# Optimization experiments

Measured on AMD Instinct MI355X. Metric: run time of the kernel, lower is better.

The kernel has to match this reference:

```python
import jax, jax.numpy as jnp
import numpy as np

B = 2          # batch size
T2 = 9         # temporal groups (b*t2 = grid_sample batch)
T3 = 27        # t1 // t2
T1 = 243       # t2 * t3
P = 17         # joints
K2 = 9         # kernel_size ** 2
C = 128        # dim_img
CH = [48, 96, 192, 384]
HW = [(96, 72), (48, 36), (24, 18), (12, 9)]
ALPHA = 0.9


def setup_inputs() -> dict:
    key = jax.random.key(0)
    ks = jax.random.split(key, 16)
    inp = {}
    N = B * T2
    for i, (c, (h, w)) in enumerate(zip(CH, HW)):
        inp[f"f{i}"] = jax.random.normal(ks[i], (N, c, h, w), jnp.float32)
    inp["query"] = jax.random.normal(ks[4], (B, T1, P * K2, C), jnp.float32)
    # key holds normalized grid coords in [-1, 1]
    inp["key"] = jax.random.uniform(ks[5], (N, T3, P * K2, 2), jnp.float32) * 2.0 - 1.0
    inp["value"] = jax.random.normal(ks[6], (B, T1, P, C), jnp.float32)
    s = 0.05
    inp["w_off"] = jax.random.normal(ks[7], (2, C), jnp.float32) * s
    inp["b_off"] = jnp.zeros((2,), jnp.float32)
    inp["w_attn"] = jax.random.normal(ks[8], (2, C), jnp.float32) * s
    inp["b_attn"] = jnp.zeros((2,), jnp.float32)
    for i, c in enumerate(CH):
        inp[f"we{i}"] = jax.random.normal(ks[9 + i], (C, c), jnp.float32) * s
        inp[f"be{i}"] = jnp.zeros((C,), jnp.float32)
    inp["conv_w"] = jax.random.normal(ks[13], (C, C, K2), jnp.float32) * s
    inp["conv_b"] = jnp.zeros((C,), jnp.float32)
    return inp


def _grid_sample(img, grid):
    """Bilinear grid_sample, align_corners=False, zero padding.
    img: [N, C, H, W]; grid: [N, Hg, Wg, 2] in [-1,1] (x=width, y=height).
    Returns [N, Hg, Wg, C] (channels-last for the following 1x1 conv)."""
    N, Cin, H, W = img.shape
    gx, gy = grid[..., 0], grid[..., 1]
    ix = ((gx + 1.0) * W - 1.0) * 0.5
    iy = ((gy + 1.0) * H - 1.0) * 0.5
    ix0 = jnp.floor(ix); iy0 = jnp.floor(iy)
    wx1 = ix - ix0; wx0 = 1.0 - wx1
    wy1 = iy - iy0; wy0 = 1.0 - wy1
    bidx = jnp.arange(N)[:, None, None]

    def gather(yy, xx):
        yi = yy.astype(jnp.int32); xi = xx.astype(jnp.int32)
        valid = (yi >= 0) & (yi < H) & (xi >= 0) & (xi < W)
        yc = jnp.clip(yi, 0, H - 1); xc = jnp.clip(xi, 0, W - 1)
        v = img[bidx, :, yc, xc]  # [N, Hg, Wg, C]
        return v * valid[..., None].astype(img.dtype)

    out = (gather(iy0, ix0) * (wy0 * wx0)[..., None]
           + gather(iy0, ix0 + 1.0) * (wy0 * wx1)[..., None]
           + gather(iy0 + 1.0, ix0) * (wy1 * wx0)[..., None]
           + gather(iy0 + 1.0, ix0 + 1.0) * (wy1 * wx1)[..., None])
    return out


def reference(f0, f1, f2, f3, query, key, value,
              w_off, b_off, w_attn, b_attn,
              we0, be0, we1, be1, we2, be2, we3, be3,
              conv_w, conv_b):
    b, t1, p, c = value.shape            # [B, 243, 17, 128]
    t3 = key.shape[1]                    # 27
    t2 = t1 // t3                        # 9

    # learned offsets per query location, squashed by tanh
    off = jnp.tanh(jnp.einsum('btqc,oc->btqo', query, w_off) + b_off)   # [b,t1,153,2]
    # per-joint softmax weights, tiled over the k^2 kernel taps
    aw = jax.nn.softmax(jnp.einsum('btpc,oc->btpo', value, w_attn) + b_attn, axis=-1)  # [b,t1,17,2]
    aw = jnp.tile(aw, (1, 1, K2, 1))                                     # [b,t1,153,2]

    sp = (off * aw).reshape(b * t2, t3, p * K2, 2)
    sampling_positions = key + sp                                        # [b*t2, 27, 153, 2]

    fmaps = (f0, f1, f2, f3)
    ws = (we0, we1, we2, we3)
    bs = (be0, be1, be2, be3)
    feats = []
    for f, w, bb in zip(fmaps, ws, bs):
        g = _grid_sample(f, sampling_positions)                          # [b*t2, 27, 153, C_in]
        e = jnp.einsum('nhwc,oc->nhwo', g, w) + bb                        # 1x1 conv embed -> 128
        feats.append(e.reshape(b, t2 * t3, p * K2, C))                    # [b, 243, 153, 128]
    new_query = jnp.mean(jnp.stack(feats, axis=-2), axis=-2)             # fuse 4 levels
    new_query = (1.0 - ALPHA) * new_query + ALPHA * query

    # grouped-by-position conv1d over the k^2 taps (full-width kernel -> length 1)
    x = new_query.reshape(b, t1, p, K2, c)                               # 'b t (p k) c'
    new_value = jnp.einsum('btpkc,ock->btpo', x, conv_w) + conv_b        # [b, 243, 17, 128]
    return (new_query, new_value, sampling_positions)
```

## Files before the change

kernel.cpp:

```cpp
#include <hip/hip_runtime.h>
#include <hip/hip_bf16.h>

static constexpr int NQ_SIZE = 9517824;
static constexpr int NV_SIZE = 1057536;
static constexpr int NPOS    = 74358;
static constexpr int M_CONV  = 8262;

static constexpr long E0_OFF = 0;
static constexpr long E1_OFF = 15925248;
static constexpr long E2_OFF = E1_OFF + 3981312;
static constexpr long E3_OFF = E2_OFF + 995328;
static constexpr long E_END  = E3_OFF + 248832;

static constexpr int SEG_F3  = 36;
static constexpr int SEG_F2  = SEG_F3 + 126;
static constexpr int SEG_F1  = SEG_F2 + 486;
static constexpr int SEG_F0  = SEG_F1 + 1944;
static constexpr int SEG_CT  = SEG_F0 + 576;
static constexpr int SEG_SP  = SEG_CT + 486;
static constexpr int PREP_GRID = SEG_SP;

typedef __attribute__((ext_vector_type(8))) short short8;
typedef __attribute__((ext_vector_type(4))) float floatx4;

__device__ __forceinline__ float bf2f(unsigned short u) {
    union { unsigned int i; float f; } v; v.i = ((unsigned)u) << 16; return v.f;
}
__device__ __forceinline__ unsigned short f2bf_rne(float f) {
    union { float f; unsigned int i; } v; v.f = f;
    unsigned int u = v.i;
    u += 0x7fffu + ((u >> 16) & 1u);
    return (unsigned short)(u >> 16);
}

__global__ __launch_bounds__(256) void prep_k(
    const float* __restrict__ f0, const float* __restrict__ f1,
    const float* __restrict__ f2, const float* __restrict__ f3,
    const float* __restrict__ we0, const float* __restrict__ we1,
    const float* __restrict__ we2, const float* __restrict__ we3,
    const float* __restrict__ conv_w, unsigned short* __restrict__ convT2,
    const float* __restrict__ query, const float* __restrict__ value,
    const float* __restrict__ key,
    const float* __restrict__ w_off, const float* __restrict__ b_off,
    const float* __restrict__ w_attn, const float* __restrict__ b_attn,
    float* __restrict__ samp, unsigned short* __restrict__ Ebase)
{
    const int bid = blockIdx.x;
    const int tid = threadIdx.x;

    if (bid < SEG_F0) {
        __shared__ unsigned short As[64][40];
        __shared__ unsigned short Bs[128][40];

        const float* A; const float* W; unsigned short* Eo;
        int M, K, m0;
        if (bid < SEG_F3) {
            int n = bid >> 1, t = bid & 1;
            M = 108; K = 384; A = f3 + (long)n * 384 * 108; W = we3;
            Eo = Ebase + E3_OFF + (long)n * 108 * 128; m0 = t * 64;
        } else if (bid < SEG_F2) {
            int r = bid - SEG_F3; int n = r / 7, t = r - n * 7;
            M = 432; K = 192; A = f2 + (long)n * 192 * 432; W = we2;
            Eo = Ebase + E2_OFF + (long)n * 432 * 128; m0 = t * 64;
        } else if (bid < SEG_F1) {
            int r = bid - SEG_F2; int n = r / 27, t = r - n * 27;
            M = 1728; K = 96; A = f1 + (long)n * 96 * 1728; W = we1;
            Eo = Ebase + E1_OFF + (long)n * 1728 * 128; m0 = t * 64;
        } else {
            int r = bid - SEG_F1; int n = r / 108, t = r - n * 108;
            M = 6912; K = 48; A = f0 + (long)n * 48 * 6912; W = we0;
            Eo = Ebase + E0_OFF + (long)n * 6912 * 128; m0 = t * 64;
        }

        const int lane = tid & 63;
        const int wave = tid >> 6;
        const int wm = (wave & 1) * 32;
        const int wn = (wave >> 1) * 64;
        const int l15  = lane & 15;
        const int quad = lane >> 4;

        floatx4 acc[2][4];
        #pragma unroll
        for (int i = 0; i < 2; ++i)
            #pragma unroll
            for (int j = 0; j < 4; ++j) acc[i][j] = (floatx4){0.f, 0.f, 0.f, 0.f};

        const int sak = tid >> 3;
        const int sam = (tid & 7) << 3;
        const int sbo = tid >> 1;
        const int sbk = (tid & 1) << 4;

        float4 av0, av1, bv0, bv1, bv2, bv3;
        auto fetch = [&](int k0) {
            av0 = (float4){0,0,0,0}; av1 = (float4){0,0,0,0};
            if (k0 + sak < K) {
                const float* p = A + (long)(k0 + sak) * M + m0 + sam;
                if (m0 + sam + 7 < M) {
                    av0 = *(const float4*)p;
                    av1 = *(const float4*)(p + 4);
                } else if (m0 + sam < M) {
                    float tmp[8] = {0,0,0,0,0,0,0,0};
                    int nv_ = M - (m0 + sam);
                    for (int i = 0; i < 8; ++i) if (i < nv_) tmp[i] = p[i];
                    av0 = (float4){tmp[0], tmp[1], tmp[2], tmp[3]};
                    av1 = (float4){tmp[4], tmp[5], tmp[6], tmp[7]};
                }
            }
            bv0 = (float4){0,0,0,0}; bv1 = bv0; bv2 = bv0; bv3 = bv0;
            if (k0 + sbk < K) {
                const float* wp = W + (long)sbo * K + k0 + sbk;
                bv0 = *(const float4*)wp;
                bv1 = *(const float4*)(wp + 4);
                bv2 = *(const float4*)(wp + 8);
                bv3 = *(const float4*)(wp + 12);
            }
        };
        fetch(0);

        for (int k0 = 0; k0 < K; k0 += 32) {
            {
                float tmp[8] = {av0.x, av0.y, av0.z, av0.w, av1.x, av1.y, av1.z, av1.w};
                #pragma unroll
                for (int i = 0; i < 8; ++i)
                    As[sam + i][sak] = f2bf_rne(tmp[i]);
            }
            {
                unsigned short t[16];
                float tmp[16] = {bv0.x, bv0.y, bv0.z, bv0.w, bv1.x, bv1.y, bv1.z, bv1.w,
                                 bv2.x, bv2.y, bv2.z, bv2.w, bv3.x, bv3.y, bv3.z, bv3.w};
                #pragma unroll
                for (int i = 0; i < 16; ++i) t[i] = f2bf_rne(tmp[i]);
                *(uint4*)&Bs[sbo][sbk]     = *(const uint4*)&t[0];
                *(uint4*)&Bs[sbo][sbk + 8] = *(const uint4*)&t[8];
            }
            __syncthreads();
            if (k0 + 32 < K) fetch(k0 + 32);

            short8 af[2], bfr[4];
            #pragma unroll
            for (int mt = 0; mt < 2; ++mt)
                af[mt] = *(const short8*)&As[wm + mt * 16 + l15][quad * 8];
            #pragma unroll
            for (int nt = 0; nt < 4; ++nt)
                bfr[nt] = *(const short8*)&Bs[wn + nt * 16 + l15][quad * 8];
            #pragma unroll
            for (int mt = 0; mt < 2; ++mt)
                #pragma unroll
                for (int nt = 0; nt < 4; ++nt)
                    acc[mt][nt] = __builtin_amdgcn_mfma_f32_16x16x32_bf16(
                        af[mt], bfr[nt], acc[mt][nt], 0, 0, 0);
            __syncthreads();
        }

        #pragma unroll
        for (int mt = 0; mt < 2; ++mt) {
            #pragma unroll
            for (int nt = 0; nt < 4; ++nt) {
                int col = wn + nt * 16 + l15;
                #pragma unroll
                for (int r = 0; r < 4; ++r) {
                    int m = m0 + wm + mt * 16 + quad * 4 + r;
                    if (m < M)
                        Eo[(long)m * 128 + col] = f2bf_rne(acc[mt][nt][r]);
                }
            }
        }
    } else if (bid < SEG_CT) {
        int idx = (bid - SEG_F0) * 256 + tid;
        if (idx < 147456) {
            int o = idx / 1152, kk = idx - o * 1152;
            int k2 = kk >> 7, c = kk & 127;
            convT2[idx] = f2bf_rne(conv_w[o * 1152 + c * 9 + k2]);
        }
    } else {
        const int bt1 = bid - SEG_CT;
        const int b  = bt1 / 243, t1 = bt1 - b * 243;
        const int t2 = t1 / 27,  t3 = t1 - t2 * 27;
        const int n  = b * 9 + t2;
        __shared__ float logit[17][2];
        __shared__ float aw[17][2];

        if (tid < 34) {
            int p = tid >> 1, o = tid & 1;
            const float* vrow = value + ((long)bt1 * 17 + p) * 128;
            const float* wrow = w_attn + o * 128;
            float s = 0.f;
            for (int c = 0; c < 128; c += 4) {
                float4 v = *(const float4*)(vrow + c);
                float4 w = *(const float4*)(wrow + c);
                s += v.x * w.x + v.y * w.y + v.z * w.z + v.w * w.w;
            }
            logit[p][o] = s + b_attn[o];
        }
        __syncthreads();
        if (tid < 17) {
            float l0 = logit[tid][0], l1 = logit[tid][1];
            float mx = fmaxf(l0, l1);
            float e0 = expf(l0 - mx), e1 = expf(l1 - mx);
            float inv = 1.f / (e0 + e1);
            aw[tid][0] = e0 * inv; aw[tid][1] = e1 * inv;
        }
        __syncthreads();
        for (int j = tid; j < 306; j += 256) {
            int q = j >> 1, o = j & 1;
            const float* qrow = query + ((long)bt1 * 153 + q) * 128;
            const float* wrow = w_off + o * 128;
            float s = 0.f;
            for (int c = 0; c < 128; c += 4) {
                float4 v = *(const float4*)(qrow + c);
                float4 w = *(const float4*)(wrow + c);
                s += v.x * w.x + v.y * w.y + v.z * w.z + v.w * w.w;
            }
            float off = tanhf(s + b_off[o]);
            float sp = off * aw[q % 17][o];
            long kidx = (((long)n * 27 + t3) * 153 + q) * 2 + o;
            samp[kidx] = key[kidx] + sp;
        }
    }
}

__global__ __launch_bounds__(256) void gather_k(
    const unsigned short* __restrict__ Ebase,
    const float* __restrict__ samp, const float* __restrict__ query,
    const float* __restrict__ be0, const float* __restrict__ be1,
    const float* __restrict__ be2, const float* __restrict__ be3,
    float* __restrict__ nq)
{
    const int tid = threadIdx.x;
    const int pos = blockIdx.x * 8 + (tid >> 5);
    if (pos >= NPOS) return;
    const int c4 = (tid & 31) << 2;
    const int bt1 = pos / 153, q = pos - bt1 * 153;
    const int b  = bt1 / 243, t1 = bt1 - b * 243;
    const int t2 = t1 / 27,  t3 = t1 - t2 * 27;
    const int n  = b * 9 + t2;
    const long sbase = (((long)n * 27 + t3) * 153 + q) * 2;
    const float gx = samp[sbase], gy = samp[sbase + 1];

    float ax = 0.f, ay = 0.f, az = 0.f, aww = 0.f;
    const long Eoffs[4] = {E0_OFF, E1_OFF, E2_OFF, E3_OFF};
    const int Hs[4] = {96, 48, 24, 12}, Wd[4] = {72, 36, 18, 9};
    #pragma unroll
    for (int l = 0; l < 4; ++l) {
        const int H = Hs[l], W = Wd[l];
        const unsigned short* E = Ebase + Eoffs[l] + (long)n * H * W * 128 + c4;
        float ix = ((gx + 1.f) * (float)W - 1.f) * 0.5f;
        float iy = ((gy + 1.f) * (float)H - 1.f) * 0.5f;
        float fx0 = floorf(ix), fy0 = floorf(iy);
        int x0 = (int)fx0, y0 = (int)fy0;
        int x1 = x0 + 1, y1 = y0 + 1;
        float wx1 = ix - fx0, wx0 = 1.f - wx1;
        float wy1 = iy - fy0, wy0 = 1.f - wy1;
        float w00 = wy0 * wx0, w01 = wy0 * wx1, w10 = wy1 * wx0, w11 = wy1 * wx1;
        bool vy0 = (unsigned)y0 < (unsigned)H, vy1 = (unsigned)y1 < (unsigned)H;
        bool vx0 = (unsigned)x0 < (unsigned)W, vx1 = (unsigned)x1 < (unsigned)W;
        if (vy0 && vx0) { ushort4 v = *(const ushort4*)(E + ((long)y0 * W + x0) * 128);
            ax = fmaf(w00, bf2f(v.x), ax); ay = fmaf(w00, bf2f(v.y), ay);
            az = fmaf(w00, bf2f(v.z), az); aww = fmaf(w00, bf2f(v.w), aww); }
        if (vy0 && vx1) { ushort4 v = *(const ushort4*)(E + ((long)y0 * W + x1) * 128);
            ax = fmaf(w01, bf2f(v.x), ax); ay = fmaf(w01, bf2f(v.y), ay);
            az = fmaf(w01, bf2f(v.z), az); aww = fmaf(w01, bf2f(v.w), aww); }
        if (vy1 && vx0) { ushort4 v = *(const ushort4*)(E + ((long)y1 * W + x0) * 128);
            ax = fmaf(w10, bf2f(v.x), ax); ay = fmaf(w10, bf2f(v.y), ay);
            az = fmaf(w10, bf2f(v.z), az); aww = fmaf(w10, bf2f(v.w), aww); }
        if (vy1 && vx1) { ushort4 v = *(const ushort4*)(E + ((long)y1 * W + x1) * 128);
            ax = fmaf(w11, bf2f(v.x), ax); ay = fmaf(w11, bf2f(v.y), ay);
            az = fmaf(w11, bf2f(v.z), az); aww = fmaf(w11, bf2f(v.w), aww); }
    }
    float bsx = be0[c4]     + be1[c4]     + be2[c4]     + be3[c4];
    float bsy = be0[c4 + 1] + be1[c4 + 1] + be2[c4 + 1] + be3[c4 + 1];
    float bsz = be0[c4 + 2] + be1[c4 + 2] + be2[c4 + 2] + be3[c4 + 2];
    float bsw = be0[c4 + 3] + be1[c4 + 3] + be2[c4 + 3] + be3[c4 + 3];
    float mx = 0.25f * (ax + bsx), my = 0.25f * (ay + bsy);
    float mz = 0.25f * (az + bsz), mw = 0.25f * (aww + bsw);
    const long qi = ((long)bt1 * 153 + q) * 128 + c4;
    float4 qv = *(const float4*)(query + qi);
    float4 o;
    o.x = 0.1f * mx + 0.9f * qv.x;
    o.y = 0.1f * my + 0.9f * qv.y;
    o.z = 0.1f * mz + 0.9f * qv.z;
    o.w = 0.1f * mw + 0.9f * qv.w;
    *(float4*)(nq + qi) = o;
}

__global__ __launch_bounds__(256) void conv_mfma_k(
    const float* __restrict__ nq, const unsigned short* __restrict__ convT2,
    const float* __restrict__ conv_b, float* __restrict__ nv)
{
    __shared__ unsigned short As[64][40];
    __shared__ unsigned short Bs[64][40];

    const int tid  = threadIdx.x;
    const int lane = tid & 63;
    const int wave = tid >> 6;
    const int wm = (wave & 1) * 32;
    const int wn = (wave >> 1) * 32;
    const int m0 = blockIdx.x * 64;
    const int n0 = blockIdx.y * 64;
    const int l15  = lane & 15;
    const int quad = lane >> 4;

    floatx4 acc[2][2];
    #pragma unroll
    for (int i = 0; i < 2; ++i)
        #pragma unroll
        for (int j = 0; j < 2; ++j) acc[i][j] = (floatx4){0.f, 0.f, 0.f, 0.f};

    const int am = tid >> 2;
    const int ak = (tid & 3) << 3;
    const int bn = tid & 63;
    const int bk = (tid >> 6) << 3;

    float4 a0, a1; uint4 bv;
    auto fetch = [&](int k0) {
        a0 = (float4){0,0,0,0}; a1 = (float4){0,0,0,0};
        int row = m0 + am;
        if (row < M_CONV) {
            const float* p = nq + (long)row * 1152 + k0 + ak;
            a0 = *(const float4*)p;
            a1 = *(const float4*)(p + 4);
        }
        bv = *(const uint4*)(convT2 + (long)(n0 + bn) * 1152 + k0 + bk);
    };
    fetch(0);

    for (int k0 = 0; k0 < 1152; k0 += 32) {
        unsigned short* dst = &As[am][ak];
        dst[0] = f2bf_rne(a0.x); dst[1] = f2bf_rne(a0.y);
        dst[2] = f2bf_rne(a0.z); dst[3] = f2bf_rne(a0.w);
        dst[4] = f2bf_rne(a1.x); dst[5] = f2bf_rne(a1.y);
        dst[6] = f2bf_rne(a1.z); dst[7] = f2bf_rne(a1.w);
        *(uint4*)&Bs[bn][bk] = bv;
        __syncthreads();
        if (k0 + 32 < 1152) fetch(k0 + 32);

        short8 af[2], bfr[2];
        #pragma unroll
        for (int mt = 0; mt < 2; ++mt)
            af[mt] = *(const short8*)&As[wm + mt * 16 + l15][quad * 8];
        #pragma unroll
        for (int nt = 0; nt < 2; ++nt)
            bfr[nt] = *(const short8*)&Bs[wn + nt * 16 + l15][quad * 8];
        #pragma unroll
        for (int mt = 0; mt < 2; ++mt)
            #pragma unroll
            for (int nt = 0; nt < 2; ++nt)
                acc[mt][nt] = __builtin_amdgcn_mfma_f32_16x16x32_bf16(
                    af[mt], bfr[nt], acc[mt][nt], 0, 0, 0);
        __syncthreads();
    }

    #pragma unroll
    for (int mt = 0; mt < 2; ++mt) {
        #pragma unroll
        for (int nt = 0; nt < 2; ++nt) {
            int col = n0 + wn + nt * 16 + l15;
            float bias = conv_b[col];
            #pragma unroll
            for (int r = 0; r < 4; ++r) {
                int row = m0 + wm + mt * 16 + quad * 4 + r;
                if (row < M_CONV)
                    nv[(long)row * 128 + col] = acc[mt][nt][r] + bias;
            }
        }
    }
}

extern "C" void kernel_launch(void* const* d_in, const int* in_sizes, int n_in,
                              void* d_out, int out_size, void* d_ws, size_t ws_size,
                              hipStream_t stream) {
    const float* f0     = (const float*)d_in[0];
    const float* f1     = (const float*)d_in[1];
    const float* f2     = (const float*)d_in[2];
    const float* f3     = (const float*)d_in[3];
    const float* query  = (const float*)d_in[4];
    const float* key    = (const float*)d_in[5];
    const float* value  = (const float*)d_in[6];
    const float* w_off  = (const float*)d_in[7];
    const float* b_off  = (const float*)d_in[8];
    const float* w_attn = (const float*)d_in[9];
    const float* b_attn = (const float*)d_in[10];
    const float* we0    = (const float*)d_in[11];
    const float* be0    = (const float*)d_in[12];
    const float* we1    = (const float*)d_in[13];
    const float* be1    = (const float*)d_in[14];
    const float* we2    = (const float*)d_in[15];
    const float* be2    = (const float*)d_in[16];
    const float* we3    = (const float*)d_in[17];
    const float* be3    = (const float*)d_in[18];
    const float* conv_w = (const float*)d_in[19];
    const float* conv_b = (const float*)d_in[20];

    float* out  = (float*)d_out;
    float* nq   = out;
    float* nv   = out + NQ_SIZE;
    float* samp = out + NQ_SIZE + NV_SIZE;

    unsigned short* Ebase  = (unsigned short*)d_ws;
    unsigned short* convT2 = Ebase + E_END;

    prep_k<<<PREP_GRID, 256, 0, stream>>>(
        f0, f1, f2, f3, we0, we1, we2, we3, conv_w, convT2,
        query, value, key, w_off, b_off, w_attn, b_attn, samp, Ebase);

    gather_k<<<(NPOS + 7) / 8, 256, 0, stream>>>(Ebase, samp, query, be0, be1, be2, be3, nq);

    conv_mfma_k<<<dim3(130, 2), 256, 0, stream>>>(nq, convT2, conv_b, nv);
}
```

Measured before the change: 246.9 us.

## Fuse bilinear gather with grouped conv via LDS tile, restructure embed GEMM A-load

Merges the gather and conv kernels into one kernel per (b,t1) row. The row's 153x128 new_query tile is kept in LDS as bf16 and fed directly to MFMA against the conv weights, which removes the conv kernel's re-read of new_query from global memory and one launch. The embedding GEMM in prep now loads A fragments straight from global into registers, dropping the As LDS transpose, with each wave owning 16 rows across all 128 columns. The trade-offs are only 486 blocks of 512 threads, a conv stage that wastes MFMA lanes on 17 useful rows out of 32, and uncoalesced strided A loads.

```diff
diff --git a/kernel.cpp b/kernel.cpp
--- a/kernel.cpp
+++ b/kernel.cpp
@@ -3,8 +3,6 @@
 
 static constexpr int NQ_SIZE = 9517824;
 static constexpr int NV_SIZE = 1057536;
-static constexpr int NPOS    = 74358;
-static constexpr int M_CONV  = 8262;
 
 static constexpr long E0_OFF = 0;
 static constexpr long E1_OFF = 15925248;
@@ -31,6 +29,12 @@
     unsigned int u = v.i;
     u += 0x7fffu + ((u >> 16) & 1u);
     return (unsigned short)(u >> 16);
+}
+__device__ __forceinline__ short8 pack8(const float* t) {
+    union { unsigned short u[8]; short8 s; } r;
+    #pragma unroll
+    for (int i = 0; i < 8; ++i) r.u[i] = f2bf_rne(t[i]);
+    return r.s;
 }
 
 __global__ __launch_bounds__(256) void prep_k(
@@ -49,7 +53,6 @@
     const int tid = threadIdx.x;
 
     if (bid < SEG_F0) {
-        __shared__ unsigned short As[64][40];
         __shared__ unsigned short Bs[128][40];
 
         const float* A; const float* W; unsigned short* Eo;
@@ -74,38 +77,19 @@
 
         const int lane = tid & 63;
         const int wave = tid >> 6;
-        const int wm = (wave & 1) * 32;
-        const int wn = (wave >> 1) * 64;
         const int l15  = lane & 15;
         const int quad = lane >> 4;
-
-        floatx4 acc[2][4];
+        const int mg   = m0 + wave * 16 + l15;
+
+        floatx4 acc[8];
         #pragma unroll
-        for (int i = 0; i < 2; ++i)
-            #pragma unroll
-            for (int j = 0; j < 4; ++j) acc[i][j] = (floatx4){0.f, 0.f, 0.f, 0.f};
-
-        const int sak = tid >> 3;
-        const int sam = (tid & 7) << 3;
+        for (int j = 0; j < 8; ++j) acc[j] = (floatx4){0.f, 0.f, 0.f, 0.f};
+
         const int sbo = tid >> 1;
         const int sbk = (tid & 1) << 4;
 
-        float4 av0, av1, bv0, bv1, bv2, bv3;
-        auto fetch = [&](int k0) {
-            av0 = (float4){0,0,0,0}; av1 = (float4){0,0,0,0};
-            if (k0 + sak < K) {
-                const float* p = A + (long)(k0 + sak) * M + m0 + sam;
-                if (m0 + sam + 7 < M) {
-                    av0 = *(const float4*)p;
-                    av1 = *(const float4*)(p + 4);
-                } else if (m0 + sam < M) {
-                    float tmp[8] = {0,0,0,0,0,0,0,0};
-                    int nv_ = M - (m0 + sam);
-                    for (int i = 0; i < 8; ++i) if (i < nv_) tmp[i] = p[i];
-                    av0 = (float4){tmp[0], tmp[1], tmp[2], tmp[3]};
-                    av1 = (float4){tmp[4], tmp[5], tmp[6], tmp[7]};
-                }
-            }
+        float4 bv0, bv1, bv2, bv3;
+        auto fetchB = [&](int k0) {
             bv0 = (float4){0,0,0,0}; bv1 = bv0; bv2 = bv0; bv3 = bv0;
             if (k0 + sbk < K) {
                 const float* wp = W + (long)sbo * K + k0 + sbk;
@@ -115,54 +99,48 @@
                 bv3 = *(const float4*)(wp + 12);
             }
         };
-        fetch(0);
+        fetchB(0);
 
         for (int k0 = 0; k0 < K; k0 += 32) {
+            float a_f[8];
             {
-                float tmp[8] = {av0.x, av0.y, av0.z, av0.w, av1.x, av1.y, av1.z, av1.w};
+                const int kq = k0 + quad * 8;
+                const float* ap = A + (long)kq * M + mg;
                 #pragma unroll
-                for (int i = 0; i < 8; ++i)
-                    As[sam + i][sak] = f2bf_rne(tmp[i]);
+                for (int j = 0; j < 8; ++j) {
+                    a_f[j] = 0.f;
+                    if (mg < M && kq + j < K) a_f[j] = ap[(long)j * M];
+                }
             }
             {
-                unsigned short t[16];
                 float tmp[16] = {bv0.x, bv0.y, bv0.z, bv0.w, bv1.x, bv1.y, bv1.z, bv1.w,
                                  bv2.x, bv2.y, bv2.z, bv2.w, bv3.x, bv3.y, bv3.z, bv3.w};
+                unsigned short t[16];
                 #pragma unroll
                 for (int i = 0; i < 16; ++i) t[i] = f2bf_rne(tmp[i]);
                 *(uint4*)&Bs[sbo][sbk]     = *(const uint4*)&t[0];
                 *(uint4*)&Bs[sbo][sbk + 8] = *(const uint4*)&t[8];
             }
             __syncthreads();
-            if (k0 + 32 < K) fetch(k0 + 32);
-
-            short8 af[2], bfr[4];
+            if (k0 + 32 < K) fetchB(k0 + 32);
+
+            short8 af = pack8(a_f);
             #pragma unroll
-            for (int mt = 0; mt < 2; ++mt)
-                af[mt] = *(const short8*)&As[wm + mt * 16 + l15][quad * 8];
+            for (int nt = 0; nt < 8; ++nt) {
+                short8 bf = *(const short8*)&Bs[nt * 16 + l15][quad * 8];
+                acc[nt] = __builtin_amdgcn_mfma_f32_16x16x32_bf16(af, bf, acc[nt], 0, 0, 0);
+            }
+            __syncthreads();
+        }
+
+        #pragma unroll
+        for (int nt = 0; nt < 8; ++nt) {
+            int col = nt * 16 + l15;
             #pragma unroll
-            for (int nt = 0; nt < 4; ++nt)
-                bfr[nt] = *(const short8*)&Bs[wn + nt * 16 + l15][quad * 8];
-            #pragma unroll
-            for (int mt = 0; mt < 2; ++mt)
-                #pragma unroll
-                for (int nt = 0; nt < 4; ++nt)
-                    acc[mt][nt] = __builtin_amdgcn_mfma_f32_16x16x32_bf16(
-                        af[mt], bfr[nt], acc[mt][nt], 0, 0, 0);
-            __syncthreads();
-        }
-
-        #pragma unroll
-        for (int mt = 0; mt < 2; ++mt) {
-            #pragma unroll
-            for (int nt = 0; nt < 4; ++nt) {
-                int col = wn + nt * 16 + l15;
-                #pragma unroll
-                for (int r = 0; r < 4; ++r) {
-                    int m = m0 + wm + mt * 16 + quad * 4 + r;
-                    if (m < M)
-                        Eo[(long)m * 128 + col] = f2bf_rne(acc[mt][nt][r]);
-                }
+            for (int r = 0; r < 4; ++r) {
+                int m = m0 + wave * 16 + quad * 4 + r;
+                if (m < M)
+                    Eo[(long)m * 128 + col] = f2bf_rne(acc[nt][r]);
             }
         }
     } else if (bid < SEG_CT) {
@@ -219,149 +197,117 @@
     }
 }
 
-__global__ __launch_bounds__(256) void gather_k(
+__global__ __launch_bounds__(512) void gc_k(
     const unsigned short* __restrict__ Ebase,
     const float* __restrict__ samp, const float* __restrict__ query,
     const float* __restrict__ be0, const float* __restrict__ be1,
     const float* __restrict__ be2, const float* __restrict__ be3,
-    float* __restrict__ nq)
+    const unsigned short* __restrict__ convT2, const float* __restrict__ conv_b,
+    float* __restrict__ nq, float* __restrict__ nv)
 {
+    __shared__ unsigned short nqb[153][136];
+
     const int tid = threadIdx.x;
-    const int pos = blockIdx.x * 8 + (tid >> 5);
-    if (pos >= NPOS) return;
-    const int c4 = (tid & 31) << 2;
-    const int bt1 = pos / 153, q = pos - bt1 * 153;
+    const int bt1 = blockIdx.x;
     const int b  = bt1 / 243, t1 = bt1 - b * 243;
     const int t2 = t1 / 27,  t3 = t1 - t2 * 27;
     const int n  = b * 9 + t2;
-    const long sbase = (((long)n * 27 + t3) * 153 + q) * 2;
-    const float gx = samp[sbase], gy = samp[sbase + 1];
-
-    float ax = 0.f, ay = 0.f, az = 0.f, aww = 0.f;
+
+    const int g  = tid >> 5;
+    const int c4 = (tid & 31) << 2;
     const long Eoffs[4] = {E0_OFF, E1_OFF, E2_OFF, E3_OFF};
     const int Hs[4] = {96, 48, 24, 12}, Wd[4] = {72, 36, 18, 9};
-    #pragma unroll
-    for (int l = 0; l < 4; ++l) {
-        const int H = Hs[l], W = Wd[l];
-        const unsigned short* E = Ebase + Eoffs[l] + (long)n * H * W * 128 + c4;
-        float ix = ((gx + 1.f) * (float)W - 1.f) * 0.5f;
-        float iy = ((gy + 1.f) * (float)H - 1.f) * 0.5f;
-        float fx0 = floorf(ix), fy0 = floorf(iy);
-        int x0 = (int)fx0, y0 = (int)fy0;
-        int x1 = x0 + 1, y1 = y0 + 1;
-        float wx1 = ix - fx0, wx0 = 1.f - wx1;
-        float wy1 = iy - fy0, wy0 = 1.f - wy1;
-        float w00 = wy0 * wx0, w01 = wy0 * wx1, w10 = wy1 * wx0, w11 = wy1 * wx1;
-        bool vy0 = (unsigned)y0 < (unsigned)H, vy1 = (unsigned)y1 < (unsigned)H;
-        bool vx0 = (unsigned)x0 < (unsigned)W, vx1 = (unsigned)x1 < (unsigned)W;
-        if (vy0 && vx0) { ushort4 v = *(const ushort4*)(E + ((long)y0 * W + x0) * 128);
-            ax = fmaf(w00, bf2f(v.x), ax); ay = fmaf(w00, bf2f(v.y), ay);
-            az = fmaf(w00, bf2f(v.z), az); aww = fmaf(w00, bf2f(v.w), aww); }
-        if (vy0 && vx1) { ushort4 v = *(const ushort4*)(E + ((long)y0 * W + x1) * 128);
-            ax = fmaf(w01, bf2f(v.x), ax); ay = fmaf(w01, bf2f(v.y), ay);
-            az = fmaf(w01, bf2f(v.z), az); aww = fmaf(w01, bf2f(v.w), aww); }
-        if (vy1 && vx0) { ushort4 v = *(const ushort4*)(E + ((long)y1 * W + x0) * 128);
-            ax = fmaf(w10, bf2f(v.x), ax); ay = fmaf(w10, bf2f(v.y), ay);
-            az = fmaf(w10, bf2f(v.z), az); aww = fmaf(w10, bf2f(v.w), aww); }
-        if (vy1 && vx1) { ushort4 v = *(const ushort4*)(E + ((long)y1 * W + x1) * 128);
-            ax = fmaf(w11, bf2f(v.x), ax); ay = fmaf(w11, bf2f(v.y), ay);
-            az = fmaf(w11, bf2f(v.z), az); aww = fmaf(w11, bf2f(v.w), aww); }
-    }
+
     float bsx = be0[c4]     + be1[c4]     + be2[c4]     + be3[c4];
     float bsy = be0[c4 + 1] + be1[c4 + 1] + be2[c4 + 1] + be3[c4 + 1];
     float bsz = be0[c4 + 2] + be1[c4 + 2] + be2[c4 + 2] + be3[c4 + 2];
     float bsw = be0[c4 + 3] + be1[c4 + 3] + be2[c4 + 3] + be3[c4 + 3];
-    float mx = 0.25f * (ax + bsx), my = 0.25f * (ay + bsy);
-    float mz = 0.25f * (az + bsz), mw = 0.25f * (aww + bsw);
-    const long qi = ((long)bt1 * 153 + q) * 128 + c4;
-    float4 qv = *(const float4*)(query + qi);
-    float4 o;
-    o.x = 0.1f * mx + 0.9f * qv.x;
-    o.y = 0.1f * my + 0.9f * qv.y;
-    o.z = 0.1f * mz + 0.9f * qv.z;
-    o.w = 0.1f * mw + 0.9f * qv.w;
-    *(float4*)(nq + qi) = o;
-}
-
-__global__ __launch_bounds__(256) void conv_mfma_k(
-    const float* __restrict__ nq, const unsigned short* __restrict__ convT2,
-    const float* __restrict__ conv_b, float* __restrict__ nv)
-{
-    __shared__ unsigned short As[64][40];
-    __shared__ unsigned short Bs[64][40];
-
-    const int tid  = threadIdx.x;
+
+    for (int it = 0; it < 10; ++it) {
+        const int q = it * 16 + g;
+        if (q < 153) {
+            const long sbase = (((long)n * 27 + t3) * 153 + q) * 2;
+            const float gx = samp[sbase], gy = samp[sbase + 1];
+
+            float ax = 0.f, ay = 0.f, az = 0.f, aww = 0.f;
+            #pragma unroll
+            for (int l = 0; l < 4; ++l) {
+                const int H = Hs[l], W = Wd[l];
+                const unsigned short* E = Ebase + Eoffs[l] + (long)n * H * W * 128 + c4;
+                float ix = ((gx + 1.f) * (float)W - 1.f) * 0.5f;
+                float iy = ((gy + 1.f) * (float)H - 1.f) * 0.5f;
+                float fx0 = floorf(ix), fy0 = floorf(iy);
+                int x0 = (int)fx0, y0 = (int)fy0;
+                int x1 = x0 + 1, y1 = y0 + 1;
+                float wx1 = ix - fx0, wx0 = 1.f - wx1;
+                float wy1 = iy - fy0, wy0 = 1.f - wy1;
+                float w00 = wy0 * wx0, w01 = wy0 * wx1, w10 = wy1 * wx0, w11 = wy1 * wx1;
+                bool vy0 = (unsigned)y0 < (unsigned)H, vy1 = (unsigned)y1 < (unsigned)H;
+                bool vx0 = (unsigned)x0 < (unsigned)W, vx1 = (unsigned)x1 < (unsigned)W;
+                if (vy0 && vx0) { ushort4 v = *(const ushort4*)(E + ((long)y0 * W + x0) * 128);
+                    ax = fmaf(w00, bf2f(v.x), ax); ay = fmaf(w00, bf2f(v.y), ay);
+                    az = fmaf(w00, bf2f(v.z), az); aww = fmaf(w00, bf2f(v.w), aww); }
+                if (vy0 && vx1) { ushort4 v = *(const ushort4*)(E + ((long)y0 * W + x1) * 128);
+                    ax = fmaf(w01, bf2f(v.x), ax); ay = fmaf(w01, bf2f(v.y), ay);
+                    az = fmaf(w01, bf2f(v.z), az); aww = fmaf(w01, bf2f(v.w), aww); }
+                if (vy1 && vx0) { ushort4 v = *(const ushort4*)(E + ((long)y1 * W + x0) * 128);
+                    ax = fmaf(w10, bf2f(v.x), ax); ay = fmaf(w10, bf2f(v.y), ay);
+                    az = fmaf(w10, bf2f(v.z), az); aww = fmaf(w10, bf2f(v.w), aww); }
+                if (vy1 && vx1) { ushort4 v = *(const ushort4*)(E + ((long)y1 * W + x1) * 128);
+                    ax = fmaf(w11, bf2f(v.x), ax); ay = fmaf(w11, bf2f(v.y), ay);
+                    az = fmaf(w11, bf2f(v.z), az); aww = fmaf(w11, bf2f(v.w), aww); }
+            }
+            float mx = 0.25f * (ax + bsx), my = 0.25f * (ay + bsy);
+            float mz = 0.25f * (az + bsz), mw = 0.25f * (aww + bsw);
+            const long qi = ((long)bt1 * 153 + q) * 128 + c4;
+            float4 qv = *(const float4*)(query + qi);
+            float4 o;
+            o.x = 0.1f * mx + 0.9f * qv.x;
+            o.y = 0.1f * my + 0.9f * qv.y;
+            o.z = 0.1f * mz + 0.9f * qv.z;
+            o.w = 0.1f * mw + 0.9f * qv.w;
+            *(float4*)(nq + qi) = o;
+            unsigned short t[4] = {f2bf_rne(o.x), f2bf_rne(o.y), f2bf_rne(o.z), f2bf_rne(o.w)};
+            *(uint2*)&nqb[q][c4] = *(const uint2*)t;
+        }
+    }
+    __syncthreads();
+
     const int lane = tid & 63;
     const int wave = tid >> 6;
-    const int wm = (wave & 1) * 32;
-    const int wn = (wave >> 1) * 32;
-    const int m0 = blockIdx.x * 64;
-    const int n0 = blockIdx.y * 64;
+    const int mt   = wave >> 2;
+    const int n0   = (wave & 3) * 32;
     const int l15  = lane & 15;
     const int quad = lane >> 4;
 
-    floatx4 acc[2][2];
-    #pragma unroll
-    for (int i = 0; i < 2; ++i)
-        #pragma unroll
-        for (int j = 0; j < 2; ++j) acc[i][j] = (floatx4){0.f, 0.f, 0.f, 0.f};
-
-    const int am = tid >> 2;
-    const int ak = (tid & 3) << 3;
-    const int bn = tid & 63;
-    const int bk = (tid >> 6) << 3;
-
-    float4 a0, a1; uint4 bv;
-    auto fetch = [&](int k0) {
-        a0 = (float4){0,0,0,0}; a1 = (float4){0,0,0,0};
-        int row = m0 + am;
-        if (row < M_CONV) {
-            const float* p = nq + (long)row * 1152 + k0 + ak;
-            a0 = *(const float4*)p;
-            a1 = *(const float4*)(p + 4);
-        }
-        bv = *(const uint4*)(convT2 + (long)(n0 + bn) * 1152 + k0 + bk);
-    };
-    fetch(0);
-
-    for (int k0 = 0; k0 < 1152; k0 += 32) {
-        unsigned short* dst = &As[am][ak];
-        dst[0] = f2bf_rne(a0.x); dst[1] = f2bf_rne(a0.y);
-        dst[2] = f2bf_rne(a0.z); dst[3] = f2bf_rne(a0.w);
-        dst[4] = f2bf_rne(a1.x); dst[5] = f2bf_rne(a1.y);
-        dst[6] = f2bf_rne(a1.z); dst[7] = f2bf_rne(a1.w);
-        *(uint4*)&Bs[bn][bk] = bv;
-        __syncthreads();
-        if (k0 + 32 < 1152) fetch(k0 + 32);
-
-        short8 af[2], bfr[2];
-        #pragma unroll
-        for (int mt = 0; mt < 2; ++mt)
-            af[mt] = *(const short8*)&As[wm + mt * 16 + l15][quad * 8];
-        #pragma unroll
-        for (int nt = 0; nt < 2; ++nt)
-            bfr[nt] = *(const short8*)&Bs[wn + nt * 16 + l15][quad * 8];
-        #pragma unroll
-        for (int mt = 0; mt < 2; ++mt)
-            #pragma unroll
-            for (int nt = 0; nt < 2; ++nt)
-                acc[mt][nt] = __builtin_amdgcn_mfma_f32_16x16x32_bf16(
-                    af[mt], bfr[nt], acc[mt][nt], 0, 0, 0);
-        __syncthreads();
-    }
-
-    #pragma unroll
-    for (int mt = 0; mt < 2; ++mt) {
+    floatx4 acc[2];
+    acc[0] = (floatx4){0.f, 0.f, 0.f, 0.f};
+    acc[1] = acc[0];
+
+    const int p = mt * 16 + l15;
+    for (int kt = 0; kt < 36; ++kt) {
+        const int k0 = kt * 32;
+        const int k2 = k0 >> 7;
+        const int cb = (k0 & 127) + quad * 8;
+        const int qq = (p < 17) ? (p * 9 + k2) : 0;
+        short8 af = *(const short8*)&nqb[qq][cb];
         #pragma unroll
         for (int nt = 0; nt < 2; ++nt) {
-            int col = n0 + wn + nt * 16 + l15;
-            float bias = conv_b[col];
-            #pragma unroll
-            for (int r = 0; r < 4; ++r) {
-                int row = m0 + wm + mt * 16 + quad * 4 + r;
-                if (row < M_CONV)
-                    nv[(long)row * 128 + col] = acc[mt][nt][r] + bias;
-            }
+            const int col = n0 + nt * 16 + l15;
+            short8 bf = *(const short8*)(convT2 + (long)col * 1152 + k0 + quad * 8);
+            acc[nt] = __builtin_amdgcn_mfma_f32_16x16x32_bf16(af, bf, acc[nt], 0, 0, 0);
+        }
+    }
+
+    #pragma unroll
+    for (int nt = 0; nt < 2; ++nt) {
+        const int col = n0 + nt * 16 + l15;
+        const float bias = conv_b[col];
+        #pragma unroll
+        for (int r = 0; r < 4; ++r) {
+            const int pr = mt * 16 + quad * 4 + r;
+            if (pr < 17)
+                nv[((long)bt1 * 17 + pr) * 128 + col] = acc[nt][r] + bias;
         }
     }
 }
@@ -403,7 +349,6 @@
         f0, f1, f2, f3, we0, we1, we2, we3, conv_w, convT2,
         query, value, key, w_off, b_off, w_attn, b_attn, samp, Ebase);
 
-    gather_k<<<(NPOS + 7) / 8, 256, 0, stream>>>(Ebase, samp, query, be0, be1, be2, be3, nq);
-
-    conv_mfma_k<<<dim3(130, 2), 256, 0, stream>>>(nq, convT2, conv_b, nv);
-}
+    gc_k<<<486, 512, 0, stream>>>(Ebase, samp, query, be0, be1, be2, be3,
+                                  convT2, conv_b, nq, nv);
+}
```

Result: slower. 279.6 us (+13.2%).
